# Optimization experiments

Hardware: AMD Instinct MI355X
Metric: run time of the kernel (lower is better)

## Reference

```python
import jax, jax.numpy as jnp
import numpy as np

N_HEADS = 32
N_KV = 8
HEAD_DIM = 128
EPS = 1e-5

def _rope(t, fr, fi):
    # t: [b,s,h,hd] -> pairs [b,s,h,hd/2,2]; fr/fi: [s,hd/2]
    tp = t.astype(jnp.float32).reshape(*t.shape[:-1], HEAD_DIM // 2, 2)
    a, b = tp[..., 0], tp[..., 1]
    fr = fr[None, :, None, :]
    fi = fi[None, :, None, :]
    out = jnp.stack([a * fr - b * fi, a * fi + b * fr], axis=-1)
    return out.reshape(t.shape).astype(t.dtype)

def _rmsnorm(t):
    tf = t.astype(jnp.float32)
    return (tf * jax.lax.rsqrt(jnp.mean(tf * tf, axis=-1, keepdims=True) + EPS)).astype(t.dtype)

def setup_inputs() -> dict:
    key = jax.random.key(0)
    ks = jax.random.split(key, 5)
    b, s, dim = 1, 2048, 4096
    x = jax.random.normal(ks[0], (b, s, dim), dtype=jnp.float32) * 0.02
    wq = jax.random.normal(ks[1], (dim, dim), dtype=jnp.float32) * 0.02
    wk = jax.random.normal(ks[2], (N_KV * HEAD_DIM, dim), dtype=jnp.float32) * 0.02
    wv = jax.random.normal(ks[3], (N_KV * HEAD_DIM, dim), dtype=jnp.float32) * 0.02
    wo = jax.random.normal(ks[4], (dim, dim), dtype=jnp.float32) * 0.02
    # RoPE freqs, llama-style theta=10000
    inv = 1.0 / (10000.0 ** (np.arange(0, HEAD_DIM, 2, dtype=np.float32) / HEAD_DIM))
    ang = np.outer(np.arange(s, dtype=np.float32), inv)  # [s, hd/2]
    freqs_cis = jnp.asarray(np.stack([np.cos(ang), np.sin(ang)], axis=-1))  # [s, hd/2, 2]
    # causal additive mask
    mask = jnp.where(jnp.tril(jnp.ones((s, s), dtype=bool)), 0.0, -1e30).astype(jnp.float32)
    return {"x": x, "wq": wq, "wk": wk, "wv": wv, "wo": wo,
            "freqs_cis": freqs_cis, "mask": mask, "start_pos": 0}

def reference(x, wq, wk, wv, wo, freqs_cis, mask, start_pos):
    b, s, dim = x.shape
    n_rep = N_HEADS // N_KV
    xq = jnp.einsum('bsd,ed->bse', x, wq).reshape(b, s, N_HEADS, HEAD_DIM)
    xk = jnp.einsum('bsd,ed->bse', x, wk).reshape(b, s, N_KV, HEAD_DIM)
    xv = jnp.einsum('bsd,ed->bse', x, wv).reshape(b, s, N_KV, HEAD_DIM)
    fr, fi = freqs_cis[..., 0], freqs_cis[..., 1]
    xq = _rope(xq, fr, fi)
    xk = _rope(xk, fr, fi)
    xq = _rmsnorm(xq)
    xk = _rmsnorm(xk)
    # start_pos=0 prefill: KV cache write/read is identity on xk/xv
    q = xq.transpose(0, 2, 1, 3).reshape(b, N_KV, n_rep, s, HEAD_DIM)  # grouped query heads
    k = xk.transpose(0, 2, 1, 3)  # [b, n_kv, s, hd]
    v = xv.transpose(0, 2, 1, 3)
    scores = jnp.einsum('bkrsd,bktd->bkrst', q, k) / np.sqrt(HEAD_DIM)
    scores = scores + mask[None, None, None, :, :]
    probs = jax.nn.softmax(scores, axis=-1)
    o = jnp.einsum('bkrst,bktd->bkrsd', probs, v)
    o = o.reshape(b, N_HEADS, s, HEAD_DIM).transpose(0, 2, 1, 3).reshape(b, s, dim)
    return jnp.einsum('bse,de->bsd', o, wo)
```

## Files before the change

kernel.cpp:

```cpp
#include <hip/hip_runtime.h>
#include <hip/hip_bf16.h>
#include <cstdint>
#include <cstddef>

using u16 = unsigned short;
using u32 = unsigned int;
using u64 = unsigned long long;

typedef __attribute__((ext_vector_type(8))) __bf16 bf16x8;
typedef __attribute__((ext_vector_type(4))) float f32x4;
typedef __attribute__((ext_vector_type(2))) float f32x2;
typedef __attribute__((ext_vector_type(4))) u32 u32x4;

typedef const __attribute__((address_space(1))) void* gas_ptr;
typedef __attribute__((address_space(3))) void* las_ptr;

__device__ __forceinline__ void async_cp16(const void* g, void* l) {
  __builtin_amdgcn_global_load_lds((gas_ptr)g, (las_ptr)l, 16, 0, 0);
}

__device__ __forceinline__ float bf2f(u16 u) {
  u32 v = ((u32)u) << 16;
  return __builtin_bit_cast(float, v);
}
__device__ __forceinline__ u16 f2bf(float f) {
  u32 v = __builtin_bit_cast(u32, f);
  u32 r = (v + 0x7fffu + ((v >> 16) & 1u)) >> 16;
  return (u16)r;
}

__device__ __forceinline__ f32x4 mfma16(bf16x8 a, bf16x8 b, f32x4 c) {
  return __builtin_amdgcn_mfma_f32_16x16x32_bf16(a, b, c, 0, 0, 0);
}

__global__ __launch_bounds__(256) void cvt_f32_bf16(const float* __restrict__ in,
                                                    u16* __restrict__ out, int n8) {
  int i = blockIdx.x * blockDim.x + threadIdx.x;
  int stride = gridDim.x * blockDim.x;
  for (; i < n8; i += stride) {
    const float4* p = (const float4*)(in + (size_t)i * 8);
    float4 a = p[0], b = p[1];
    union { u16 us[8]; u32x4 v; } o;
    o.us[0] = f2bf(a.x); o.us[1] = f2bf(a.y); o.us[2] = f2bf(a.z); o.us[3] = f2bf(a.w);
    o.us[4] = f2bf(b.x); o.us[5] = f2bf(b.y); o.us[6] = f2bf(b.z); o.us[7] = f2bf(b.w);
    *(u32x4*)(out + (size_t)i * 8) = o.v;
  }
}

__global__ __launch_bounds__(256) void cvt4(const float* __restrict__ x,
                                            const float* __restrict__ wq,
                                            const float* __restrict__ wk,
                                            const float* __restrict__ wv,
                                            u16* __restrict__ xb,
                                            u16* __restrict__ wqkv) {
  const int B0 = 1048576;
  const int B1 = B0 + 2097152;
  const int B2 = B1 + 524288;
  const int B3 = B2 + 524288;
  int i = blockIdx.x * blockDim.x + threadIdx.x;
  int stride = gridDim.x * blockDim.x;
  for (; i < B3; i += stride) {
    const float* src; u16* dst; int j;
    if (i < B0)      { src = x;  dst = xb;                           j = i; }
    else if (i < B1) { src = wq; dst = wqkv;                         j = i - B0; }
    else if (i < B2) { src = wk; dst = wqkv + (size_t)4096 * 4096;   j = i - B1; }
    else             { src = wv; dst = wqkv + (size_t)5120 * 4096;   j = i - B2; }
    const float4* p = (const float4*)(src + (size_t)j * 8);
    float4 a = p[0], b = p[1];
    union { u16 us[8]; u32x4 v; } o;
    o.us[0] = f2bf(a.x); o.us[1] = f2bf(a.y); o.us[2] = f2bf(a.z); o.us[3] = f2bf(a.w);
    o.us[4] = f2bf(b.x); o.us[5] = f2bf(b.y); o.us[6] = f2bf(b.z); o.us[7] = f2bf(b.w);
    *(u32x4*)(dst + (size_t)j * 8) = o.v;
  }
}

template <int MODE>
__global__ __launch_bounds__(256, 3) void gemm_bt(const u16* __restrict__ A,
                                                  const u16* __restrict__ B,
                                                  void* __restrict__ Cv,
                                                  int M, int N, int K,
                                                  u16* __restrict__ qh,
                                                  u16* __restrict__ khh,
                                                  u16* __restrict__ vt,
                                                  const float* __restrict__ freqs) {
  __shared__ __align__(16) u16 As[128 * 64];
  __shared__ __align__(16) u16 Bs[128 * 64];
  const int tid = threadIdx.x;
  const int wave = tid >> 6, lane = tid & 63;
  const int quad = lane >> 4, c16 = lane & 15;

  const int mb = M >> 7, nb = N >> 7;
  const int per_xcd_n = nb >> 3;
  const int xcd = blockIdx.x & 7, lid = blockIdx.x >> 3;
  const int m_t = lid % mb, n_local = lid / mb;
  const int m0 = m_t * 128, n0 = (xcd * per_xcd_n + n_local) * 128;

  const int wm = (wave & 1) * 64, wn = (wave >> 1) * 64;

  f32x4 acc[4][4] = {};

  const u16* Ab = A + (size_t)m0 * K;
  const u16* Bb = B + (size_t)n0 * K;

  for (int k0 = 0; k0 < K; k0 += 64) {
    __syncthreads();
#pragma unroll
    for (int i = 0; i < 4; ++i) {
      int idx = tid + 256 * i;
      int row = idx >> 3, sg = (idx & 7) ^ (row & 7);
      async_cp16(Ab + (size_t)row * K + k0 + sg * 8, As + (size_t)idx * 8);
    }
#pragma unroll
    for (int i = 0; i < 4; ++i) {
      int idx = tid + 256 * i;
      int row = idx >> 3, sg = (idx & 7) ^ (row & 7);
      async_cp16(Bb + (size_t)row * K + k0 + sg * 8, Bs + (size_t)idx * 8);
    }
    asm volatile("s_waitcnt vmcnt(0)" ::: "memory");
    __syncthreads();

    bf16x8 af[4][2], bfr[4][2];
#pragma unroll
    for (int mt = 0; mt < 4; ++mt) {
      int row = wm + mt * 16 + c16;
#pragma unroll
      for (int c = 0; c < 2; ++c)
        af[mt][c] = *(const bf16x8*)(As + row * 64 + (((c * 4 + quad) ^ (row & 7)) * 8));
    }
#pragma unroll
    for (int nt = 0; nt < 4; ++nt) {
      int row = wn + nt * 16 + c16;
#pragma unroll
      for (int c = 0; c < 2; ++c)
        bfr[nt][c] = *(const bf16x8*)(Bs + row * 64 + (((c * 4 + quad) ^ (row & 7)) * 8));
    }
#pragma unroll
    for (int c = 0; c < 2; ++c)
#pragma unroll
      for (int mt = 0; mt < 4; ++mt)
#pragma unroll
        for (int nt = 0; nt < 4; ++nt)
          acc[mt][nt] = mfma16(af[mt][c], bfr[nt][c], acc[mt][nt]);
  }

  if constexpr (MODE == 1) {
#pragma unroll
    for (int mt = 0; mt < 4; ++mt) {
#pragma unroll
      for (int nt = 0; nt < 4; ++nt) {
#pragma unroll
        for (int r = 0; r < 4; ++r) {
          int gm = m0 + wm + mt * 16 + quad * 4 + r;
          int gn = n0 + wn + nt * 16 + c16;
          ((float*)Cv)[(size_t)gm * N + gn] = acc[mt][nt][r];
        }
      }
    }
  } else {
    __syncthreads();
    float* sums = (float*)As;
    if (n0 < 5120) {
      float ss_arr[4][4];
#pragma unroll
      for (int mt = 0; mt < 4; ++mt) {
#pragma unroll
        for (int r = 0; r < 4; ++r) {
          int s = m0 + wm + mt * 16 + quad * 4 + r;
          const float* fb = freqs + (size_t)s * 128;
          float ssv = 0.0f;
#pragma unroll
          for (int nt = 0; nt < 4; ++nt) {
            int d = wn + nt * 16 + c16;
            float v = acc[mt][nt][r];
            float p = __shfl_xor(v, 1, 64);
            f32x2 ff = *(const f32x2*)(fb + (d & ~1));
            float res = (c16 & 1) ? fmaf(v, ff.x, p * ff.y)
                                  : fmaf(v, ff.x, -p * ff.y);
            acc[mt][nt][r] = res;
            ssv = fmaf(res, res, ssv);
          }
#pragma unroll
          for (int m = 1; m < 16; m <<= 1) ssv += __shfl_xor(ssv, m, 64);
          ss_arr[mt][r] = ssv;
        }
      }
      const int wn_idx = wave >> 1;
      if (c16 == 0) {
#pragma unroll
        for (int mt = 0; mt < 4; ++mt)
#pragma unroll
          for (int r = 0; r < 4; ++r)
            sums[wn_idx * 128 + wm + mt * 16 + quad * 4 + r] = ss_arr[mt][r];
      }
      __syncthreads();
      u16* outb = (n0 < 4096)
                      ? (qh + (size_t)(n0 >> 7) * M * 128)
                      : (khh + (size_t)((n0 - 4096) >> 7) * M * 128);
#pragma unroll
      for (int mt = 0; mt < 4; ++mt) {
#pragma unroll
        for (int r = 0; r < 4; ++r) {
          int rl = wm + mt * 16 + quad * 4 + r;
          float tot = ss_arr[mt][r] + sums[(wn_idx ^ 1) * 128 + rl];
          float scl = rsqrtf(tot * (1.0f / 128.0f) + 1e-5f);
          int s = m0 + rl;
#pragma unroll
          for (int nt = 0; nt < 4; ++nt)
            outb[(size_t)s * 128 + wn + nt * 16 + c16] = f2bf(acc[mt][nt][r] * scl);
        }
      }
    } else {
#pragma unroll
      for (int mt = 0; mt < 4; ++mt) {
#pragma unroll
        for (int nt = 0; nt < 4; ++nt) {
          int dv = (n0 - 5120) + wn + nt * 16 + c16;
          int s0 = m0 + wm + mt * 16 + quad * 4;
          union { u16 us[4]; u64 v; } pk;
#pragma unroll
          for (int r = 0; r < 4; ++r) pk.us[r] = f2bf(acc[mt][nt][r]);
          *(u64*)(vt + (size_t)dv * M + s0) = pk.v;
        }
      }
    }
  }
}

#define SEQ 2048
__global__ __launch_bounds__(512, 2) void attn(const u16* __restrict__ Q,
                                               const u16* __restrict__ Kh,
                                               const u16* __restrict__ VT,
                                               u16* __restrict__ O) {
  __shared__ __align__(16) u16 Ks[2][64 * 128];
  __shared__ __align__(16) u16 Vs[2][128 * 64];
  __shared__ __align__(16) u16 Ps[8][32 * 64];
  const int tid = threadIdx.x;
  const int wave = tid >> 6, lane = tid & 63;
  const int quad = lane >> 4, c16 = lane & 15;
  const int bid = blockIdx.x;
  const int hk = bid & 7;
  const int rest = bid >> 3;
  const int hq = rest & 3;
  const int p = rest >> 2;
  const int h = hk * 4 + hq;

  const int wl = wave & 3, grp = wave >> 2;
  const int qt = grp ? p : (15 - p);
  const int q0w = qt * 128 + wl * 32;
  const int kend = (15 - p) * 128 + 128;

  const float sc = 0.12751743f;
  const float B = 16.5f;
  const u16* Kb = Kh + (size_t)hk * SEQ * 128;
  const u16* Vb = VT + (size_t)hk * 128 * SEQ;

  auto stage = [&](int t0, int b) __attribute__((always_inline)) {
#pragma unroll
    for (int i = 0; i < 2; ++i) {
      int idx = tid + 512 * i;
      int row = idx >> 4, sg = (idx & 15) ^ (row & 7);
      async_cp16(Kb + (size_t)(t0 + row) * 128 + sg * 8, &Ks[b][(size_t)idx * 8]);
    }
#pragma unroll
    for (int i = 0; i < 2; ++i) {
      int idx = tid + 512 * i;
      int row = idx >> 3, sg = (idx & 7) ^ (row & 7);
      async_cp16(Vb + (size_t)row * SEQ + t0 + sg * 8, &Vs[b][(size_t)idx * 8]);
    }
  };

  bf16x8 qfr[2][4];
  const u16* qbase = Q + (size_t)h * SEQ * 128;
#pragma unroll
  for (int g = 0; g < 2; ++g)
#pragma unroll
    for (int c = 0; c < 4; ++c)
      qfr[g][c] =
          *(const bf16x8*)(qbase + (size_t)(q0w + g * 16 + c16) * 128 + c * 32 + quad * 8);

  f32x4 o_acc[2][8] = {};
  float lsum[2][4] = {};

  stage(0, 0);

#pragma unroll 1
  for (int t0 = 0; t0 < kend; t0 += 64) {
    const int cur = (t0 >> 6) & 1;
    asm volatile("s_waitcnt vmcnt(0)" ::: "memory");
    __syncthreads();
    if (t0 + 64 < kend) stage(t0 + 64, cur ^ 1);

    if (t0 < q0w + 32) {
      f32x4 sa[2][4] = {};
      __builtin_amdgcn_s_setprio(1);
#pragma unroll
      for (int ct = 0; ct < 4; ++ct) {
        int t = ct * 16 + c16;
        int tbase = t * 128;
        int tsw = t & 7;
#pragma unroll
        for (int c = 0; c < 4; ++c) {
          bf16x8 kf = *(const bf16x8*)(&Ks[cur][tbase + (((c * 4 + quad) ^ tsw) * 8)]);
          sa[0][ct] = mfma16(qfr[0][c], kf, sa[0][ct]);
          sa[1][ct] = mfma16(qfr[1][c], kf, sa[1][ct]);
        }
      }
      __builtin_amdgcn_s_setprio(0);

      const bool diag = (t0 + 64 > q0w);
      auto soft = [&](bool masked) __attribute__((always_inline)) {
#pragma unroll
        for (int g = 0; g < 2; ++g) {
#pragma unroll
          for (int r = 0; r < 4; ++r) {
            int row = g * 16 + quad * 4 + r;
            int row_q = q0w + row;
            int rbase = row * 64;
            int rsw = row & 7;
#pragma unroll
            for (int ct = 0; ct < 4; ++ct) {
              float s = sa[g][ct][r];
              float arg = fmaf(s, sc, -B);
              if (masked) {
                int t_idx = t0 + ct * 16 + c16;
                arg = (t_idx <= row_q) ? arg : -1.0e30f;
              }
              float pe = exp2f(arg);
              lsum[g][r] += pe;
              u32 pb = (__builtin_bit_cast(u32, pe) + 0x8000u) >> 16;
              Ps[wave][rbase + (((ct * 2 + (c16 >> 3)) ^ rsw) * 8) + (c16 & 7)] = (u16)pb;
            }
          }
        }
      };
      if (diag) soft(true); else soft(false);
      asm volatile("s_waitcnt lgkmcnt(0)" ::: "memory");

      __builtin_amdgcn_s_setprio(1);
#pragma unroll
      for (int tc = 0; tc < 2; ++tc) {
        bf16x8 pf[2];
#pragma unroll
        for (int g = 0; g < 2; ++g) {
          int prow = g * 16 + c16;
          pf[g] = *(const bf16x8*)(&Ps[wave][prow * 64 + (((tc * 4 + quad) ^ (prow & 7)) * 8)]);
        }
#pragma unroll
        for (int nt = 0; nt < 8; ++nt) {
          int dl = nt * 16 + c16;
          bf16x8 vf = *(const bf16x8*)(&Vs[cur][dl * 64 + (((tc * 4 + quad) ^ (dl & 7)) * 8)]);
          o_acc[0][nt] = mfma16(pf[0], vf, o_acc[0][nt]);
          o_acc[1][nt] = mfma16(pf[1], vf, o_acc[1][nt]);
        }
      }
      __builtin_amdgcn_s_setprio(0);
    }
  }

#pragma unroll
  for (int g = 0; g < 2; ++g) {
#pragma unroll
    for (int r = 0; r < 4; ++r) {
      float l = lsum[g][r];
#pragma unroll
      for (int m = 1; m < 16; m <<= 1) l += __shfl_xor(l, m, 64);
      float inv = 1.0f / l;
      int s_idx = q0w + g * 16 + quad * 4 + r;
      u16* ob = O + (size_t)s_idx * 4096 + (size_t)h * 128;
#pragma unroll
      for (int nt = 0; nt < 8; ++nt) ob[nt * 16 + c16] = f2bf(o_acc[g][nt][r] * inv);
    }
  }
}

extern "C" void kernel_launch(void* const* d_in, const int* in_sizes, int n_in,
                              void* d_out, int out_size, void* d_ws, size_t ws_size,
                              hipStream_t stream) {
  const float* x  = (const float*)d_in[0];
  const float* wq = (const float*)d_in[1];
  const float* wk = (const float*)d_in[2];
  const float* wv = (const float*)d_in[3];
  const float* wo = (const float*)d_in[4];
  const float* fr = (const float*)d_in[5];
  float* out = (float*)d_out;

  const size_t S = 2048, D = 4096, KV = 1024, NQKV = D + 2 * KV;
  u16* p = (u16*)d_ws;
  u16* xb   = p; p += S * D;
  u16* wqkv = p; p += NQKV * D;
  u16* qh   = p; p += S * D;
  u16* khh  = p; p += S * KV;
  u16* vt   = p; p += KV * S;
  u16* ob   = p; p += S * D;
  u16* wob = wqkv;

  cvt4<<<dim3(2048), dim3(256), 0, stream>>>(x, wq, wk, wv, xb, wqkv);

  gemm_bt<2><<<dim3((S / 128) * (NQKV / 128)), dim3(256), 0, stream>>>(
      xb, wqkv, nullptr, (int)S, (int)NQKV, (int)D, qh, khh, vt, fr);

  cvt_f32_bf16<<<dim3(2048), dim3(256), 0, stream>>>(wo, wob, (int)(D * D / 8));

  attn<<<dim3(256), dim3(512), 0, stream>>>(qh, khh, vt, ob);

  gemm_bt<1><<<dim3((S / 128) * (D / 128)), dim3(256), 0, stream>>>(
      ob, wob, (void*)out, (int)S, (int)D, (int)D,
      nullptr, nullptr, nullptr, nullptr);
}
```

Measured before the change: 459.6 us.

## Process paired causal q-tiles sequentially with 16-row waves for higher occupancy

Before, each block's 8 waves covered two 128-row query tiles at once, 32 rows per wave, and every wave walked the key range of the longer tile. Now all 8 waves take one tile (16 rows each) and the block handles the two paired tiles in two sequential phases, each stopping at its own causal end. This halves per-wave accumulator and Q fragment registers and the P scratch, and launch bounds rise to 4 blocks per CU to use the headroom. In exchange, each K/V tile loaded into LDS now feeds 16 query rows per wave instead of 32, adding LDS traffic, and phase boundaries add extra barriers.

Result: slower. 478.8 us (+4.2%).

```diff
diff --git a/kernel.cpp b/kernel.cpp
--- a/kernel.cpp
+++ b/kernel.cpp
@@ -227,13 +227,13 @@
 }
 
 #define SEQ 2048
-__global__ __launch_bounds__(512, 2) void attn(const u16* __restrict__ Q,
+__global__ __launch_bounds__(512, 4) void attn(const u16* __restrict__ Q,
                                                const u16* __restrict__ Kh,
                                                const u16* __restrict__ VT,
                                                u16* __restrict__ O) {
   __shared__ __align__(16) u16 Ks[2][64 * 128];
   __shared__ __align__(16) u16 Vs[2][128 * 64];
-  __shared__ __align__(16) u16 Ps[8][32 * 64];
+  __shared__ __align__(16) u16 Ps[8][16 * 64];
   const int tid = threadIdx.x;
   const int wave = tid >> 6, lane = tid & 63;
   const int quad = lane >> 4, c16 = lane & 15;
@@ -244,15 +244,11 @@
   const int p = rest >> 2;
   const int h = hk * 4 + hq;
 
-  const int wl = wave & 3, grp = wave >> 2;
-  const int qt = grp ? p : (15 - p);
-  const int q0w = qt * 128 + wl * 32;
-  const int kend = (15 - p) * 128 + 128;
-
   const float sc = 0.12751743f;
   const float B = 16.5f;
   const u16* Kb = Kh + (size_t)hk * SEQ * 128;
   const u16* Vb = VT + (size_t)hk * 128 * SEQ;
+  const u16* qbase = Q + (size_t)h * SEQ * 128;
 
   auto stage = [&](int t0, int b) __attribute__((always_inline)) {
 #pragma unroll
@@ -269,106 +265,98 @@
     }
   };
 
-  bf16x8 qfr[2][4];
-  const u16* qbase = Q + (size_t)h * SEQ * 128;
-#pragma unroll
-  for (int g = 0; g < 2; ++g)
+#pragma unroll 1
+  for (int ph = 0; ph < 2; ++ph) {
+    const int qt = ph ? p : (15 - p);
+    const int q0w = qt * 128 + wave * 16;
+    const int kend = qt * 128 + 128;
+
+    bf16x8 qfr[4];
 #pragma unroll
     for (int c = 0; c < 4; ++c)
-      qfr[g][c] =
-          *(const bf16x8*)(qbase + (size_t)(q0w + g * 16 + c16) * 128 + c * 32 + quad * 8);
-
-  f32x4 o_acc[2][8] = {};
-  float lsum[2][4] = {};
-
-  stage(0, 0);
+      qfr[c] = *(const bf16x8*)(qbase + (size_t)(q0w + c16) * 128 + c * 32 + quad * 8);
+
+    f32x4 o_acc[8] = {};
+    float lsum[4] = {};
+
+    __syncthreads();
+    stage(0, 0);
 
 #pragma unroll 1
-  for (int t0 = 0; t0 < kend; t0 += 64) {
-    const int cur = (t0 >> 6) & 1;
-    asm volatile("s_waitcnt vmcnt(0)" ::: "memory");
-    __syncthreads();
-    if (t0 + 64 < kend) stage(t0 + 64, cur ^ 1);
-
-    if (t0 < q0w + 32) {
-      f32x4 sa[2][4] = {};
-      __builtin_amdgcn_s_setprio(1);
-#pragma unroll
-      for (int ct = 0; ct < 4; ++ct) {
-        int t = ct * 16 + c16;
-        int tbase = t * 128;
-        int tsw = t & 7;
-#pragma unroll
-        for (int c = 0; c < 4; ++c) {
-          bf16x8 kf = *(const bf16x8*)(&Ks[cur][tbase + (((c * 4 + quad) ^ tsw) * 8)]);
-          sa[0][ct] = mfma16(qfr[0][c], kf, sa[0][ct]);
-          sa[1][ct] = mfma16(qfr[1][c], kf, sa[1][ct]);
-        }
-      }
-      __builtin_amdgcn_s_setprio(0);
-
-      const bool diag = (t0 + 64 > q0w);
-      auto soft = [&](bool masked) __attribute__((always_inline)) {
-#pragma unroll
-        for (int g = 0; g < 2; ++g) {
+    for (int t0 = 0; t0 < kend; t0 += 64) {
+      const int cur = (t0 >> 6) & 1;
+      asm volatile("s_waitcnt vmcnt(0)" ::: "memory");
+      __syncthreads();
+      if (t0 + 64 < kend) stage(t0 + 64, cur ^ 1);
+
+      if (t0 < q0w + 16) {
+        f32x4 sa[4] = {};
+        __builtin_amdgcn_s_setprio(1);
+#pragma unroll
+        for (int ct = 0; ct < 4; ++ct) {
+          int t = ct * 16 + c16;
+          int tbase = t * 128;
+          int tsw = t & 7;
+#pragma unroll
+          for (int c = 0; c < 4; ++c) {
+            bf16x8 kf = *(const bf16x8*)(&Ks[cur][tbase + (((c * 4 + quad) ^ tsw) * 8)]);
+            sa[ct] = mfma16(qfr[c], kf, sa[ct]);
+          }
+        }
+        __builtin_amdgcn_s_setprio(0);
+
+        const bool diag = (t0 + 64 > q0w);
+        auto soft = [&](bool masked) __attribute__((always_inline)) {
 #pragma unroll
           for (int r = 0; r < 4; ++r) {
-            int row = g * 16 + quad * 4 + r;
+            int row = quad * 4 + r;
             int row_q = q0w + row;
             int rbase = row * 64;
             int rsw = row & 7;
 #pragma unroll
             for (int ct = 0; ct < 4; ++ct) {
-              float s = sa[g][ct][r];
+              float s = sa[ct][r];
               float arg = fmaf(s, sc, -B);
               if (masked) {
                 int t_idx = t0 + ct * 16 + c16;
                 arg = (t_idx <= row_q) ? arg : -1.0e30f;
               }
               float pe = exp2f(arg);
-              lsum[g][r] += pe;
+              lsum[r] += pe;
               u32 pb = (__builtin_bit_cast(u32, pe) + 0x8000u) >> 16;
               Ps[wave][rbase + (((ct * 2 + (c16 >> 3)) ^ rsw) * 8) + (c16 & 7)] = (u16)pb;
             }
           }
-        }
-      };
-      if (diag) soft(true); else soft(false);
-      asm volatile("s_waitcnt lgkmcnt(0)" ::: "memory");
-
-      __builtin_amdgcn_s_setprio(1);
-#pragma unroll
-      for (int tc = 0; tc < 2; ++tc) {
-        bf16x8 pf[2];
-#pragma unroll
-        for (int g = 0; g < 2; ++g) {
-          int prow = g * 16 + c16;
-          pf[g] = *(const bf16x8*)(&Ps[wave][prow * 64 + (((tc * 4 + quad) ^ (prow & 7)) * 8)]);
-        }
-#pragma unroll
-        for (int nt = 0; nt < 8; ++nt) {
-          int dl = nt * 16 + c16;
-          bf16x8 vf = *(const bf16x8*)(&Vs[cur][dl * 64 + (((tc * 4 + quad) ^ (dl & 7)) * 8)]);
-          o_acc[0][nt] = mfma16(pf[0], vf, o_acc[0][nt]);
-          o_acc[1][nt] = mfma16(pf[1], vf, o_acc[1][nt]);
-        }
-      }
-      __builtin_amdgcn_s_setprio(0);
-    }
-  }
-
-#pragma unroll
-  for (int g = 0; g < 2; ++g) {
+        };
+        if (diag) soft(true); else soft(false);
+        asm volatile("s_waitcnt lgkmcnt(0)" ::: "memory");
+
+        __builtin_amdgcn_s_setprio(1);
+#pragma unroll
+        for (int tc = 0; tc < 2; ++tc) {
+          int prow = c16;
+          bf16x8 pf = *(const bf16x8*)(&Ps[wave][prow * 64 + (((tc * 4 + quad) ^ (prow & 7)) * 8)]);
+#pragma unroll
+          for (int nt = 0; nt < 8; ++nt) {
+            int dl = nt * 16 + c16;
+            bf16x8 vf = *(const bf16x8*)(&Vs[cur][dl * 64 + (((tc * 4 + quad) ^ (dl & 7)) * 8)]);
+            o_acc[nt] = mfma16(pf, vf, o_acc[nt]);
+          }
+        }
+        __builtin_amdgcn_s_setprio(0);
+      }
+    }
+
 #pragma unroll
     for (int r = 0; r < 4; ++r) {
-      float l = lsum[g][r];
+      float l = lsum[r];
 #pragma unroll
       for (int m = 1; m < 16; m <<= 1) l += __shfl_xor(l, m, 64);
       float inv = 1.0f / l;
-      int s_idx = q0w + g * 16 + quad * 4 + r;
+      int s_idx = q0w + quad * 4 + r;
       u16* ob = O + (size_t)s_idx * 4096 + (size_t)h * 128;
 #pragma unroll
-      for (int nt = 0; nt < 8; ++nt) ob[nt * 16 + c16] = f2bf(o_acc[g][nt][r] * inv);
+      for (int nt = 0; nt < 8; ++nt) ob[nt * 16 + c16] = f2bf(o_acc[nt][r] * inv);
     }
   }
 }
```
